# Kernel optimization log

Measured on AMD Instinct MI355X. Metric: run time of the kernel, lower is better.

The kernel has to match this reference:

```python
import jax, jax.numpy as jnp
import numpy as np

N, D_IN, D_OUT, Q_DIM = 4096, 256, 256, 64


def _xavier(key, shape):
    fan_in, fan_out = shape[-2], shape[-1]
    bound = float(np.sqrt(6.0 / (fan_in + fan_out)))
    return jax.random.uniform(key, shape, jnp.float32, -bound, bound)


def setup_inputs() -> dict:
    key = jax.random.key(0)
    k_x, k_q, k_w, k_b = jax.random.split(key, 4)
    x = jax.random.normal(k_x, (N, D_IN), jnp.float32)
    query_vectors = jax.random.normal(k_q, (N, Q_DIM), jnp.float32)
    W_1 = _xavier(k_w, (Q_DIM, D_IN, D_OUT))  # xavier over last two dims (matches torch on 3D)
    b_1 = _xavier(k_b, (Q_DIM, D_OUT))
    return {"x": x, "query_vectors": query_vectors, "W_1": W_1, "b_1": b_1}


def reference(x, query_vectors, W_1, b_1):
    # Per-sample dynamic weight: W[n] = sum_d q[n,d] * W_1[d]; then x[n] @ W[n] + q[n] @ b_1.
    # Fused single contraction avoids materializing the [n, i, o] tensor; same math.
    out = jnp.einsum('ni,nd,dio->no', x, query_vectors, W_1)
    out = out + query_vectors @ b_1
    return out
```

## Files before the change

### kernel.cpp

```cpp
#include <hip/hip_runtime.h>
#include <stdint.h>


typedef _Float16 f16;
typedef f16 f16x8 __attribute__((ext_vector_type(8)));
typedef float f32x16 __attribute__((ext_vector_type(16)));

#define QDIM 64

__device__ __forceinline__ void gl_lds16(const void* g, void* s) {
  __builtin_amdgcn_global_load_lds(
      (const __attribute__((address_space(1))) void*)(uintptr_t)g,
      (__attribute__((address_space(3))) void*)(uint32_t)(uintptr_t)s,
      16, 0, 0);
}

#define XFRAG(DST, PTR)                                      \
  do {                                                       \
    float4 a_ = *(const float4*)(PTR);                       \
    float4 b_ = *(const float4*)((PTR) + 4);                 \
    f16x8 h_;                                                \
    h_[0] = (f16)a_.x; h_[1] = (f16)a_.y; h_[2] = (f16)a_.z; \
    h_[3] = (f16)a_.w; h_[4] = (f16)b_.x; h_[5] = (f16)b_.y; \
    h_[6] = (f16)b_.z; h_[7] = (f16)b_.w;                    \
    DST = h_;                                                \
  } while (0)

__global__ __launch_bounds__(256) void prep(const float* __restrict__ W,
                                            const float* __restrict__ B1,
                                            const float* __restrict__ X,
                                            f16* __restrict__ Wt,
                                            f16* __restrict__ Xt,
                                            f16* __restrict__ Bt) {
  const int b = blockIdx.x, t = threadIdx.x;
  if (b < 512) {
    const int d = b >> 3, grp = b & 7;
#pragma unroll
    for (int r = 0; r < 4; ++r) {
      const int u = (r << 8) + t;
      const int ibq = u >> 8;
      const int o = u & 255;
      const int ib = (grp << 2) + ibq;
      f16x8 h;
#pragma unroll
      for (int j = 0; j < 8; ++j)
        h[j] = (f16)W[((size_t)d * 256 + (ib << 3) + j) * 256 + o];
      const int ncg = o >> 5, c = o & 31, ic = ib >> 1, hb = ib & 1;
      *(f16x8*)((char*)Wt + ((((size_t)ncg * 64 + d) * 16 + ic) << 10) +
                (hb << 9) + (c << 4)) = h;
    }
  } else if (b < 576) {
    const int mb = b - 512;
#pragma unroll
    for (int rep = 0; rep < 8; ++rep) {
      const int u = (rep << 8) + t;
      const int row = u & 63, ish = u >> 6;
      const float* src = X + ((size_t)((mb << 6) + row)) * 256 + (ish << 3);
      f16x8 h;
      XFRAG(h, src);
      *(f16x8*)((char*)Xt + ((((size_t)mb * 16 + (ish >> 1)) * 2 + (ish & 1)) << 10) +
                (row << 4)) = h;
    }
  } else {
#pragma unroll
    for (int kb = 0; kb < 8; ++kb) {
      const float* src = B1 + ((size_t)kb << 3) * 256 + t;
      f16x8 h;
#pragma unroll
      for (int j = 0; j < 8; ++j) h[j] = (f16)src[(size_t)j << 8];
      *(f16x8*)((char*)Bt + (((size_t)(t >> 5) * 4 + (kb >> 1)) << 10) +
                ((kb & 1) << 9) + ((t & 31) << 4)) = h;
    }
  }
}

__global__ __launch_bounds__(512, 2) void mlp_main(const float* __restrict__ Q,
                                                   const f16* __restrict__ Wt,
                                                   const f16* __restrict__ Xt,
                                                   const f16* __restrict__ Bt,
                                                   float* __restrict__ P) {
  __shared__ __align__(16) char sw0[16384];
  __shared__ __align__(16) char sw1[16384];

  const int bid = blockIdx.x;
  const int nc = bid & 3;
  const int ks = (bid >> 2) & 7;
  const int mb = bid >> 5;
  const int t = threadIdx.x;
  const int w = t >> 6;
  const int wn = w & 1;
  const int wm = w >> 1;
  const int l = t & 63;
  const int l31 = l & 31;
  const int hf = l >> 5;

  const int dlo = ks << 3;
  const int st = mb & 7;

  const char* gW = (const char*)Wt + ((size_t)nc << 21) + (l << 4);

  const char* xB = (const char*)Xt + ((size_t)((mb << 2) + wm) << 15) +
                   (hf << 10) + (l31 << 4);

  f16 qr0[8], qr1[8];
  {
    const float* qp0 = Q + ((size_t)((mb << 8) + (wm << 6) + l31)) * QDIM + dlo;
    const float* qp1 = qp0 + (size_t)32 * QDIM;
#pragma unroll
    for (int dt = 0; dt < 8; ++dt) {
      qr0[dt] = (f16)qp0[(dt + st) & 7];
      qr1[dt] = (f16)qp1[(dt + st) & 7];
    }
  }

  f32x16 acc0, acc1;
#pragma unroll
  for (int r = 0; r < 16; ++r) { acc0[r] = 0.f; acc1[r] = 0.f; }

  f16x8 xf[16];

#define STAGE2(H, DABS, SBUF)                                              \
  do {                                                                     \
    gl_lds16(gW + ((size_t)(DABS) << 14) + ((((H) << 3) + w) << 10),       \
             (SBUF) + ((w << 1) << 10) + (l << 4));                        \
    gl_lds16(gW + ((size_t)1 << 20) + ((size_t)(DABS) << 14) +             \
                 ((((H) << 3) + w) << 10),                                 \
             (SBUF) + (((w << 1) + 1) << 10) + (l << 4));                  \
  } while (0)

#define LOADXF(H)                                                          \
  do {                                                                     \
    _Pragma("unroll")                                                      \
    for (int k2 = 0; k2 < 8; ++k2) {                                       \
      xf[k2 * 2 + 0] = *(const f16x8*)(xB + ((((H) << 3) + k2) << 11));    \
      xf[k2 * 2 + 1] =                                                     \
          *(const f16x8*)(xB + ((((H) << 3) + k2) << 11) + (1 << 9));      \
    }                                                                      \
  } while (0)

#define CSTEP(DT, SBUF)                                                    \
  do {                                                                     \
    const f16 qa_ = qr0[DT], qb_ = qr1[DT];                                \
    _Pragma("unroll")                                                      \
    for (int k2 = 0; k2 < 8; ++k2) {                                       \
      f16x8 bf_ = *(const f16x8*)((SBUF) + (((k2 << 1) | wn) << 10) +      \
                                  (l << 4));                               \
      acc0 = __builtin_amdgcn_mfma_f32_32x32x16_f16(xf[k2 * 2 + 0] * qa_,  \
                                                    bf_, acc0, 0, 0, 0);   \
      acc1 = __builtin_amdgcn_mfma_f32_32x32x16_f16(xf[k2 * 2 + 1] * qb_,  \
                                                    bf_, acc1, 0, 0, 0);   \
    }                                                                      \
  } while (0)

  STAGE2(0, dlo + (st & 7), sw0);
  LOADXF(0);
  __syncthreads();

#pragma unroll
  for (int h = 0; h < 2; ++h) {
#pragma unroll
    for (int dt = 0; dt < 8; ++dt) {
      const int step = (h << 3) + dt;
      if (step < 15) {
        const int hn = (step + 1) >> 3, dtn = (step + 1) & 7;
        const int dabs = dlo + ((dtn + st) & 7);
        if (step & 1) STAGE2(hn, dabs, sw0); else STAGE2(hn, dabs, sw1);
      }
      if (step & 1) CSTEP(dt, sw1); else CSTEP(dt, sw0);
      __syncthreads();
    }
    if (h == 0) LOADXF(1);
  }

  if (ks == 0) {
    const int ncg = (nc << 1) + wn;
#pragma unroll
    for (int kc = 0; kc < 4; ++kc) {
      f16x8 bf = *(const f16x8*)((const char*)Bt +
          (((size_t)ncg * 4 + kc) << 10) + (hf << 9) + (l31 << 4));
      f16x8 q0, q1;
      XFRAG(q0, Q + ((size_t)((mb << 8) + (wm << 6) + l31)) * QDIM +
                (kc << 4) + (hf << 3));
      XFRAG(q1, Q + ((size_t)((mb << 8) + (wm << 6) + 32 + l31)) * QDIM +
                (kc << 4) + (hf << 3));
      acc0 = __builtin_amdgcn_mfma_f32_32x32x16_f16(q0, bf, acc0, 0, 0, 0);
      acc1 = __builtin_amdgcn_mfma_f32_32x32x16_f16(q1, bf, acc1, 0, 0, 0);
    }
  }

  float* Pg = P + ((size_t)ks << 20);
  const int colg = (nc << 6) + (wn << 5) + l31;
  const int rbase = (mb << 8) + (wm << 6);
#pragma unroll
  for (int r = 0; r < 16; ++r) {
    const int rr = (r & 3) + ((r >> 2) << 3) + (hf << 2);
    Pg[(size_t)(rbase + rr) * 256 + colg] = acc0[r];
    Pg[(size_t)(rbase + 32 + rr) * 256 + colg] = acc1[r];
  }
}

__global__ __launch_bounds__(256) void reduce8(const float* __restrict__ P,
                                               float* __restrict__ out) {
  const size_t i = (((size_t)blockIdx.x << 8) + threadIdx.x) << 2;
  float4 s = *(const float4*)(P + i);
#pragma unroll
  for (int g = 1; g < 8; ++g) {
    float4 v = *(const float4*)(P + ((size_t)g << 20) + i);
    s.x += v.x; s.y += v.y; s.z += v.z; s.w += v.w;
  }
  *(float4*)(out + i) = s;
}

extern "C" void kernel_launch(void* const* d_in, const int* in_sizes, int n_in,
                              void* d_out, int out_size, void* d_ws, size_t ws_size,
                              hipStream_t stream) {
  (void)in_sizes; (void)n_in; (void)out_size; (void)ws_size;
  const float* x  = (const float*)d_in[0];
  const float* q  = (const float*)d_in[1];
  const float* W1 = (const float*)d_in[2];
  const float* b1 = (const float*)d_in[3];
  float* out = (float*)d_out;

  f16* Wt = (f16*)d_ws;
  f16* Bt = (f16*)((char*)d_ws + ((size_t)8 << 20));
  f16* Xt = (f16*)((char*)d_ws + ((size_t)8 << 20) + 32768);
  float* P = (float*)((char*)d_ws + ((size_t)8 << 20) + 32768 + ((size_t)2 << 20));

  prep<<<577, 256, 0, stream>>>(W1, b1, x, Wt, Xt, Bt);
  mlp_main<<<512, 512, 0, stream>>>(q, Wt, Xt, Bt, P);
  reduce8<<<1024, 256, 0, stream>>>(P, out);
}
```

Measured before the change: 128.8 us.

## Triple-buffer W staging with explicit waitcnt barriers and re-split prep W transpose

The main kernel moves from double to triple LDS buffering. It issues two stages ahead and replaces __syncthreads with a raw s_waitcnt plus s_barrier, so loads for step s+2 overlap compute on step s, and it raises wave priority around the MFMA block. The prep kernel's W transpose is remapped so each wave writes one contiguous 1KB output chunk, spread over 2048 blocks instead of 512. The hand-coded vmcnt values assume a specific count of outstanding loads per stage, and the extra buffer raises LDS use to 48KB per block, which may limit occupancy at two blocks per CU.

```diff
diff --git a/kernel.cpp b/kernel.cpp
--- a/kernel.cpp
+++ b/kernel.cpp
@@ -33,24 +33,20 @@
                                             f16* __restrict__ Xt,
                                             f16* __restrict__ Bt) {
   const int b = blockIdx.x, t = threadIdx.x;
-  if (b < 512) {
-    const int d = b >> 3, grp = b & 7;
-#pragma unroll
-    for (int r = 0; r < 4; ++r) {
-      const int u = (r << 8) + t;
-      const int ibq = u >> 8;
-      const int o = u & 255;
-      const int ib = (grp << 2) + ibq;
-      f16x8 h;
-#pragma unroll
-      for (int j = 0; j < 8; ++j)
-        h[j] = (f16)W[((size_t)d * 256 + (ib << 3) + j) * 256 + o];
-      const int ncg = o >> 5, c = o & 31, ic = ib >> 1, hb = ib & 1;
-      *(f16x8*)((char*)Wt + ((((size_t)ncg * 64 + d) * 16 + ic) << 10) +
-                (hb << 9) + (c << 4)) = h;
-    }
-  } else if (b < 576) {
-    const int mb = b - 512;
+  if (b < 2048) {
+    const int w = t >> 6, l = t & 63, hf = l >> 5, c = l & 31;
+    const int g = (b << 2) + w;
+    const int ic = g & 15;
+    const int d = (g >> 4) & 63;
+    const int ncg = g >> 10;
+    const float* src = W + ((size_t)(d * 256 + (ic << 4) + (hf << 3)) << 8) +
+                       (ncg << 5) + c;
+    f16x8 h;
+#pragma unroll
+    for (int j = 0; j < 8; ++j) h[j] = (f16)src[(size_t)j << 8];
+    *(f16x8*)((char*)Wt + ((size_t)g << 10) + (hf << 9) + (c << 4)) = h;
+  } else if (b < 2112) {
+    const int mb = b - 2048;
 #pragma unroll
     for (int rep = 0; rep < 8; ++rep) {
       const int u = (rep << 8) + t;
@@ -79,8 +75,7 @@
                                                    const f16* __restrict__ Xt,
                                                    const f16* __restrict__ Bt,
                                                    float* __restrict__ P) {
-  __shared__ __align__(16) char sw0[16384];
-  __shared__ __align__(16) char sw1[16384];
+  __shared__ __align__(16) char sw[3][16384];
 
   const int bid = blockIdx.x;
   const int nc = bid & 3;
@@ -97,7 +92,7 @@
   const int dlo = ks << 3;
   const int st = mb & 7;
 
-  const char* gW = (const char*)Wt + ((size_t)nc << 21) + (l << 4);
+  const char* gW = (const char*)(Wt) + ((size_t)nc << 21) + (l << 4);
 
   const char* xB = (const char*)Xt + ((size_t)((mb << 2) + wm) << 15) +
                    (hf << 10) + (l31 << 4);
@@ -152,24 +147,33 @@
     }                                                                      \
   } while (0)
 
-  STAGE2(0, dlo + (st & 7), sw0);
   LOADXF(0);
-  __syncthreads();
+  STAGE2(0, dlo + ((0 + st) & 7), (char*)sw[0]);
+  STAGE2(0, dlo + ((1 + st) & 7), (char*)sw[1]);
 
 #pragma unroll
   for (int h = 0; h < 2; ++h) {
 #pragma unroll
     for (int dt = 0; dt < 8; ++dt) {
-      const int step = (h << 3) + dt;
-      if (step < 15) {
-        const int hn = (step + 1) >> 3, dtn = (step + 1) & 7;
-        const int dabs = dlo + ((dtn + st) & 7);
-        if (step & 1) STAGE2(hn, dabs, sw0); else STAGE2(hn, dabs, sw1);
+      const int s = (h << 3) + dt;
+      if (s == 15) {
+        __builtin_amdgcn_s_waitcnt(0x0F70);
+      } else {
+        __builtin_amdgcn_s_waitcnt(0x0F72);
       }
-      if (step & 1) CSTEP(dt, sw1); else CSTEP(dt, sw0);
-      __syncthreads();
-    }
-    if (h == 0) LOADXF(1);
+      __builtin_amdgcn_sched_barrier(0);
+      __builtin_amdgcn_s_barrier();
+      __builtin_amdgcn_sched_barrier(0);
+      if (s < 14) {
+        const int s2 = s + 2, hn = s2 >> 3, dtn = s2 & 7;
+        char* nb = (char*)sw[s2 % 3];
+        STAGE2(hn, dlo + ((dtn + st) & 7), nb);
+      }
+      __builtin_amdgcn_s_setprio(1);
+      CSTEP(dt, (const char*)sw[s % 3]);
+      __builtin_amdgcn_s_setprio(0);
+      if (s == 7) LOADXF(1);
+    }
   }
 
   if (ks == 0) {
@@ -226,7 +230,7 @@
   f16* Xt = (f16*)((char*)d_ws + ((size_t)8 << 20) + 32768);
   float* P = (float*)((char*)d_ws + ((size_t)8 << 20) + 32768 + ((size_t)2 << 20));
 
-  prep<<<577, 256, 0, stream>>>(W1, b1, x, Wt, Xt, Bt);
+  prep<<<2113, 256, 0, stream>>>(W1, b1, x, Wt, Xt, Bt);
   mlp_main<<<512, 512, 0, stream>>>(q, Wt, Xt, Bt, P);
   reduce8<<<1024, 256, 0, stream>>>(P, out);
 }
```

After: 127.0 us. About the same (-1.4%).
